# Optimization experiments

Measured on AMD Instinct MI355X. Metric: run time of the kernel, lower is better.

Reference implementation:

```python
import jax, jax.numpy as jnp
import numpy as np

S, B, C = 56, 5, 20
N = 128


def _cxcywh_to_xyxy(b):
    cx, cy, w, h = b[..., 0], b[..., 1], b[..., 2], b[..., 3]
    return jnp.stack([cx - 0.5 * w, cy - 0.5 * h, cx + 0.5 * w, cy + 0.5 * h], axis=-1)


def setup_inputs() -> dict:
    key = jax.random.key(0)
    k1, k2, k3 = jax.random.split(key, 3)
    predicts_tensor = jax.random.normal(k1, (N, S, S, B, C + 5), dtype=jnp.float32)
    targets_tensor = jax.random.uniform(k2, (N, S, S, C + 5), dtype=jnp.float32)
    anchors = jax.random.uniform(k3, (B, 2), dtype=jnp.float32)
    return {"predicts_tensor": predicts_tensor, "targets_tensor": targets_tensor, "anchors": anchors}


def reference(predicts_tensor, targets_tensor, anchors):
    p = predicts_tensor.reshape(-1, S, S, B, C + 5)
    # decode: sigmoid on cx,cy ; exp * anchor on w,h
    xy = jax.nn.sigmoid(p[..., C + 1:C + 3])
    wh = jnp.exp(p[..., C + 3:]) * anchors  # anchors [B,2] broadcasts over [...,B,2]
    p = jnp.concatenate([p[..., :C + 1], xy, wh], axis=-1)

    pb = _cxcywh_to_xyxy(p[..., C + 1:])                         # [N,S,S,B,4]
    tb = _cxcywh_to_xyxy(targets_tensor[..., C + 1:])[..., None, :]  # [N,S,S,1,4]

    # torchvision box_iou, vectorized over all cells and B boxes
    lt = jnp.maximum(pb[..., :2], tb[..., :2])
    rb = jnp.minimum(pb[..., 2:], tb[..., 2:])
    whi = jnp.clip(rb - lt, 0.0)
    inter = whi[..., 0] * whi[..., 1]
    area_p = (pb[..., 2] - pb[..., 0]) * (pb[..., 3] - pb[..., 1])
    area_t = (tb[..., 2] - tb[..., 0]) * (tb[..., 3] - tb[..., 1])
    ious = inter / (area_p + area_t - inter)                     # [N,S,S,B]

    best_idx = jnp.argmax(ious, axis=-1)                         # [N,S,S]
    pbest = jnp.take_along_axis(p, best_idx[..., None, None], axis=3)[..., 0, :]  # [N,S,S,C+5]
    pbest = pbest.at[..., 0].set(pbest[..., 0] * best_idx.astype(pbest.dtype))

    exists = targets_tensor[..., C:C + 1]
    sse = lambda a, b: jnp.sum((a - b) ** 2)  # MSELoss(reduction='sum')

    loss_xcyc = sse(exists * pbest[..., C + 1:C + 3], exists * targets_tensor[..., C + 1:C + 3])
    p_wh = pbest[..., C + 3:]
    p_wh = jnp.sign(p_wh) * jnp.sqrt(jnp.abs(p_wh) + 1e-6)
    loss_wh = sse(exists * p_wh, exists * targets_tensor[..., C + 3:])
    loss_cls = sse(exists * pbest[..., :C], exists * targets_tensor[..., :C])
    loss_obj = sse(exists * pbest[..., C:C + 1], exists * targets_tensor[..., C:C + 1])
    noobj = 1.0 - exists
    loss_noobj = sse(noobj * pbest[..., C:C + 1], noobj * targets_tensor[..., C:C + 1])

    return loss_xcyc + loss_wh + loss_cls + loss_noobj + loss_obj
```

## Files before the change

kernel.cpp:

```cpp
#include <hip/hip_runtime.h>

constexpr int S_   = 56;
constexpr int B_   = 5;
constexpr int C_   = 20;
constexpr int N_   = 128;
constexpr int CELLS = N_ * S_ * S_;
constexpr int PSTR  = B_ * (C_ + 5);
constexpr int TSTR  = C_ + 5;

constexpr int CPB    = 64;
constexpr int NBLK   = CELLS / CPB;
constexpr int PRED_B = CPB * PSTR * 4;

__device__ __forceinline__ void gload_lds16(const char* g, char* l) {
    __builtin_amdgcn_global_load_lds(
        (const __attribute__((address_space(1))) void*)g,
        (__attribute__((address_space(3))) void*)l,
        16, 0, 0);
}

__global__ __launch_bounds__(64) void yolo_loss_kernel(
    const float* __restrict__ pred,
    const float* __restrict__ targ,
    const float* __restrict__ anch,
    float* __restrict__ part)
{
    __shared__ char lds[PRED_B];

    const int lane  = threadIdx.x;
    const int cell0 = blockIdx.x * CPB;
    const int cell  = cell0 + lane;

    const char* gp = (const char*)(pred + (size_t)cell0 * PSTR);
    #pragma unroll
    for (int it = 0; it < 31; ++it)
        gload_lds16(gp + it * 1024 + lane * 16, lds + it * 1024);
    if (lane < 16)
        gload_lds16(gp + 31744 + lane * 16, lds + 31744);

    const float* __restrict__ tp = targ + (size_t)cell * TSTR;
    float t[TSTR];
    #pragma unroll
    for (int k = 0; k < TSTR; ++k) t[k] = tp[k];

    float aw[B_], ah[B_];
    #pragma unroll
    for (int b = 0; b < B_; ++b) { aw[b] = anch[2 * b]; ah[b] = anch[2 * b + 1]; }

    const float tcx = t[C_ + 1], tcy = t[C_ + 2];
    const float tw  = t[C_ + 3], th  = t[C_ + 4];
    const float tx0 = tcx - 0.5f * tw, ty0 = tcy - 0.5f * th;
    const float tx1 = tcx + 0.5f * tw, ty1 = tcy + 0.5f * th;
    const float area_t = tw * th;

    __syncthreads();

    const float* pc = (const float*)lds + (size_t)lane * PSTR;

    float best_iou = -1.f;
    int   best_b = 0;
    float bcx = 0.f, bcy = 0.f, bw = 0.f, bh = 0.f;

    #pragma unroll
    for (int b = 0; b < B_; ++b) {
        const float rcx = pc[b * TSTR + C_ + 1];
        const float rcy = pc[b * TSTR + C_ + 2];
        const float rw  = pc[b * TSTR + C_ + 3];
        const float rh  = pc[b * TSTR + C_ + 4];

        const float cx = __builtin_amdgcn_rcpf(1.f + __expf(-rcx));
        const float cy = __builtin_amdgcn_rcpf(1.f + __expf(-rcy));
        const float w  = __expf(rw) * aw[b];
        const float h  = __expf(rh) * ah[b];

        const float x0 = cx - 0.5f * w, y0 = cy - 0.5f * h;
        const float x1 = cx + 0.5f * w, y1 = cy + 0.5f * h;

        float wi = fminf(x1, tx1) - fmaxf(x0, tx0);
        float hi = fminf(y1, ty1) - fmaxf(y0, ty0);
        wi = fmaxf(wi, 0.f);
        hi = fmaxf(hi, 0.f);
        const float inter = wi * hi;
        const float iou = inter * __builtin_amdgcn_rcpf(w * h + area_t - inter);

        const bool better = iou > best_iou;
        best_iou = better ? iou : best_iou;
        best_b   = better ? b   : best_b;
        bcx = better ? cx : bcx;
        bcy = better ? cy : bcy;
        bw  = better ? w  : bw;
        bh  = better ? h  : bh;
    }

    const float* pb = pc + best_b * TSTR;

    float acc = 0.f;
    #pragma unroll
    for (int k = 0; k < C_; ++k) {
        float v = pb[k];
        if (k == 0) v *= (float)best_b;
        const float d = v - t[k];
        acc = fmaf(d, d, acc);
    }

    float d;
    d = bcx - tcx; acc = fmaf(d, d, acc);
    d = bcy - tcy; acc = fmaf(d, d, acc);

    d = sqrtf(bw + 1e-6f) - tw; acc = fmaf(d, d, acc);
    d = sqrtf(bh + 1e-6f) - th; acc = fmaf(d, d, acc);

    const float e    = t[C_];
    const float ne   = 1.f - e;
    const float dobj = pb[C_] - e;
    float local = e * e * acc + (e * e + ne * ne) * (dobj * dobj);

    #pragma unroll
    for (int off = 32; off > 0; off >>= 1)
        local += __shfl_down(local, off, 64);

    if (lane == 0)
        part[blockIdx.x] = local;
}

__global__ __launch_bounds__(1024) void finalize_kernel(
    const float* __restrict__ part, float* __restrict__ out)
{
    float v = 0.f;
    for (int i = threadIdx.x; i < NBLK; i += 1024)
        v += part[i];

    #pragma unroll
    for (int off = 32; off > 0; off >>= 1)
        v += __shfl_down(v, off, 64);

    __shared__ float ws[16];
    if ((threadIdx.x & 63) == 0) ws[threadIdx.x >> 6] = v;
    __syncthreads();
    if (threadIdx.x < 16) {
        float x = ws[threadIdx.x];
        #pragma unroll
        for (int off = 8; off > 0; off >>= 1)
            x += __shfl_down(x, off, 16);
        if (threadIdx.x == 0) out[0] = x;
    }
}

extern "C" void kernel_launch(void* const* d_in, const int* in_sizes, int n_in,
                              void* d_out, int out_size, void* d_ws, size_t ws_size,
                              hipStream_t stream) {
    const float* pred = (const float*)d_in[0];
    const float* targ = (const float*)d_in[1];
    const float* anch = (const float*)d_in[2];
    float* out  = (float*)d_out;
    float* part = (float*)d_ws;

    yolo_loss_kernel<<<NBLK, CPB, 0, stream>>>(pred, targ, anch, part);
    finalize_kernel<<<1, 1024, 0, stream>>>(part, out);
}
```

Baseline: 305.6 us.

## Double-buffer LDS staging of pred and target groups across four cell groups per block

Each block now handles four 64-cell groups and alternates between two LDS buffers. The next group's global-to-LDS loads are issued while the current group is computed, and explicit vmcnt waits sequence the buffers. Target rows are also staged into LDS with coalesced 16-byte loads instead of per-lane strided register loads. This roughly doubles LDS per block and cuts resident blocks per CU, so latency hiding now depends on in-block prefetch rather than on many concurrent blocks.

```diff
diff --git a/kernel.cpp b/kernel.cpp
--- a/kernel.cpp
+++ b/kernel.cpp
@@ -8,9 +8,12 @@
 constexpr int PSTR  = B_ * (C_ + 5);
 constexpr int TSTR  = C_ + 5;
 
-constexpr int CPB    = 64;
-constexpr int NBLK   = CELLS / CPB;
-constexpr int PRED_B = CPB * PSTR * 4;
+constexpr int GC    = 64;
+constexpr int GPB   = 4;
+constexpr int NBLK  = CELLS / (GC * GPB);
+constexpr int GP_B  = GC * PSTR * 4;
+constexpr int GT_B  = GC * TSTR * 4;
+constexpr int GRP_B = GP_B + GT_B;
 
 __device__ __forceinline__ void gload_lds16(const char* g, char* l) {
     __builtin_amdgcn_global_load_lds(
@@ -19,43 +22,35 @@
         16, 0, 0);
 }
 
-__global__ __launch_bounds__(64) void yolo_loss_kernel(
-    const float* __restrict__ pred,
-    const float* __restrict__ targ,
-    const float* __restrict__ anch,
-    float* __restrict__ part)
-{
-    __shared__ char lds[PRED_B];
+#define WAITVM(N) asm volatile("s_waitcnt vmcnt(" #N ")" ::: "memory")
 
-    const int lane  = threadIdx.x;
-    const int cell0 = blockIdx.x * CPB;
-    const int cell  = cell0 + lane;
-
-    const char* gp = (const char*)(pred + (size_t)cell0 * PSTR);
+__device__ __forceinline__ void stage_group(const float* __restrict__ pred,
+                                            const float* __restrict__ targ,
+                                            int g, char* buf, int lane) {
+    const char* gp = (const char*)(pred + (size_t)g * GC * PSTR);
+    const char* gt = (const char*)(targ + (size_t)g * GC * TSTR);
     #pragma unroll
     for (int it = 0; it < 31; ++it)
-        gload_lds16(gp + it * 1024 + lane * 16, lds + it * 1024);
+        gload_lds16(gp + it * 1024 + lane * 16, buf + it * 1024);
     if (lane < 16)
-        gload_lds16(gp + 31744 + lane * 16, lds + 31744);
+        gload_lds16(gp + 31744 + lane * 16, buf + 31744);
+    #pragma unroll
+    for (int it = 0; it < 6; ++it)
+        gload_lds16(gt + it * 1024 + lane * 16, buf + GP_B + it * 1024);
+    if (lane < 16)
+        gload_lds16(gt + 6144 + lane * 16, buf + GP_B + 6144);
+}
 
-    const float* __restrict__ tp = targ + (size_t)cell * TSTR;
-    float t[TSTR];
-    #pragma unroll
-    for (int k = 0; k < TSTR; ++k) t[k] = tp[k];
+__device__ __forceinline__ float cell_loss(const char* buf, int lane,
+                                           const float* aw, const float* ah) {
+    const float* pc = (const float*)buf + (size_t)lane * PSTR;
+    const float* tp = (const float*)(buf + GP_B) + (size_t)lane * TSTR;
 
-    float aw[B_], ah[B_];
-    #pragma unroll
-    for (int b = 0; b < B_; ++b) { aw[b] = anch[2 * b]; ah[b] = anch[2 * b + 1]; }
-
-    const float tcx = t[C_ + 1], tcy = t[C_ + 2];
-    const float tw  = t[C_ + 3], th  = t[C_ + 4];
+    const float tcx = tp[C_ + 1], tcy = tp[C_ + 2];
+    const float tw  = tp[C_ + 3], th  = tp[C_ + 4];
     const float tx0 = tcx - 0.5f * tw, ty0 = tcy - 0.5f * th;
     const float tx1 = tcx + 0.5f * tw, ty1 = tcy + 0.5f * th;
     const float area_t = tw * th;
-
-    __syncthreads();
-
-    const float* pc = (const float*)lds + (size_t)lane * PSTR;
 
     float best_iou = -1.f;
     int   best_b = 0;
@@ -99,7 +94,7 @@
     for (int k = 0; k < C_; ++k) {
         float v = pb[k];
         if (k == 0) v *= (float)best_b;
-        const float d = v - t[k];
+        const float d = v - tp[k];
         acc = fmaf(d, d, acc);
     }
 
@@ -110,17 +105,52 @@
     d = sqrtf(bw + 1e-6f) - tw; acc = fmaf(d, d, acc);
     d = sqrtf(bh + 1e-6f) - th; acc = fmaf(d, d, acc);
 
-    const float e    = t[C_];
+    const float e    = tp[C_];
     const float ne   = 1.f - e;
     const float dobj = pb[C_] - e;
-    float local = e * e * acc + (e * e + ne * ne) * (dobj * dobj);
+    return e * e * acc + (e * e + ne * ne) * (dobj * dobj);
+}
+
+__global__ __launch_bounds__(64) void yolo_loss_kernel(
+    const float* __restrict__ pred,
+    const float* __restrict__ targ,
+    const float* __restrict__ anch,
+    float* __restrict__ part)
+{
+    __shared__ char lds[2 * GRP_B];
+
+    const int lane = threadIdx.x;
+    const int g0   = blockIdx.x * GPB;
+
+    float aw[B_], ah[B_];
+    #pragma unroll
+    for (int b = 0; b < B_; ++b) { aw[b] = anch[2 * b]; ah[b] = anch[2 * b + 1]; }
+
+    stage_group(pred, targ, g0 + 0, lds,         lane);
+    stage_group(pred, targ, g0 + 1, lds + GRP_B, lane);
+
+    float total = 0.f;
+
+    WAITVM(39);
+    total += cell_loss(lds,         lane, aw, ah);
+    stage_group(pred, targ, g0 + 2, lds,         lane);
+
+    WAITVM(39);
+    total += cell_loss(lds + GRP_B, lane, aw, ah);
+    stage_group(pred, targ, g0 + 3, lds + GRP_B, lane);
+
+    WAITVM(39);
+    total += cell_loss(lds,         lane, aw, ah);
+
+    WAITVM(0);
+    total += cell_loss(lds + GRP_B, lane, aw, ah);
 
     #pragma unroll
     for (int off = 32; off > 0; off >>= 1)
-        local += __shfl_down(local, off, 64);
+        total += __shfl_down(total, off, 64);
 
     if (lane == 0)
-        part[blockIdx.x] = local;
+        part[blockIdx.x] = total;
 }
 
 __global__ __launch_bounds__(1024) void finalize_kernel(
@@ -155,6 +185,6 @@
     float* out  = (float*)d_out;
     float* part = (float*)d_ws;
 
-    yolo_loss_kernel<<<NBLK, CPB, 0, stream>>>(pred, targ, anch, part);
+    yolo_loss_kernel<<<NBLK, 64, 0, stream>>>(pred, targ, anch, part);
     finalize_kernel<<<1, 1024, 0, stream>>>(part, out);
 }
```

Result: no change. 304.8 us (-0.3%).
